# Optimization experiments

Hardware: AMD Instinct MI355X
Metric: run time of the kernel (lower is better)

Reference implementation:

```python
import jax, jax.numpy as jnp
import numpy as np

H = 1024      # hidden_size
L = 2         # num_layers
B = 4096      # batch_size (acts as sequential time axis)
IN = 33       # LSTM input size (17 raw + 8 ip-embed + 8 port-embed)


def setup_inputs() -> dict:
    key = jax.random.key(0)
    ks = jax.random.split(key, 16)
    s = 0.02
    return {
        "x": jax.random.normal(ks[0], (B, 17), dtype=jnp.float32),
        "ip": jax.random.randint(ks[1], (B, 8), 0, 256),
        "port": jax.random.randint(ks[2], (B, 2), 0, 70000),
        "hidden": jnp.zeros((L, 1, H), dtype=jnp.float32),
        "cell": jnp.zeros((L, 1, H), dtype=jnp.float32),
        "ip_emb": jax.random.normal(ks[3], (256, 1), dtype=jnp.float32) * s,
        "port_emb": jax.random.normal(ks[4], (70000, 4), dtype=jnp.float32) * s,
        "W_ih0": jax.random.normal(ks[5], (4 * H, IN), dtype=jnp.float32) * s,
        "W_hh0": jax.random.normal(ks[6], (4 * H, H), dtype=jnp.float32) * s,
        "b_ih0": jax.random.normal(ks[7], (4 * H,), dtype=jnp.float32) * s,
        "b_hh0": jax.random.normal(ks[8], (4 * H,), dtype=jnp.float32) * s,
        "W_ih1": jax.random.normal(ks[9], (4 * H, H), dtype=jnp.float32) * s,
        "W_hh1": jax.random.normal(ks[10], (4 * H, H), dtype=jnp.float32) * s,
        "b_ih1": jax.random.normal(ks[11], (4 * H,), dtype=jnp.float32) * s,
        "b_hh1": jax.random.normal(ks[12], (4 * H,), dtype=jnp.float32) * s,
    }


def reference(x, ip, port, hidden, cell, ip_emb, port_emb,
              W_ih0, W_hh0, b_ih0, b_hh0, W_ih1, W_hh1, b_ih1, b_hh1):
    # embedding lookups + concat -> [B, 33]
    ip_e = ip_emb[ip].reshape(B, -1)        # [B, 8]
    port_e = port_emb[port].reshape(B, -1)  # [B, 8]
    xin = jnp.concatenate((x, ip_e, port_e), axis=1)  # [B, 33]

    Wih = (W_ih0, W_ih1)
    Whh = (W_hh0, W_hh1)
    bih = (b_ih0, b_ih1)
    bhh = (b_hh0, b_hh1)

    h0 = hidden[:, 0]  # [L, H]
    c0 = cell[:, 0]    # [L, H]

    def step(carry, xt):
        h, c = carry
        inp = xt
        hs, cs = [], []
        for l in range(L):  # fixed small layer loop
            gates = Wih[l] @ inp + bih[l] + Whh[l] @ h[l] + bhh[l]  # [4H]
            i, f, g, o = jnp.split(gates, 4)  # PyTorch gate order: i,f,g,o
            i = jax.nn.sigmoid(i)
            f = jax.nn.sigmoid(f)
            g = jnp.tanh(g)
            o = jax.nn.sigmoid(o)
            c_new = f * c[l] + i * g
            h_new = o * jnp.tanh(c_new)
            hs.append(h_new)
            cs.append(c_new)
            inp = h_new
        return (jnp.stack(hs), jnp.stack(cs)), jax.nn.relu(inp)

    (hf, cf), outputs = jax.lax.scan(step, (h0, c0), xin)
    return outputs, (hf[:, None, :], cf[:, None, :])
```

## Files before the change

### kernel.cpp

```cpp
#include <hip/hip_runtime.h>
#include <hip/hip_fp16.h>
#include <math.h>

#define Hn 1024
#define Bn 4096
#define INW 33
#define OUTS (Bn * Hn)
#define TPB 512
#define ROWP 1024

typedef _Float16 half2v __attribute__((ext_vector_type(2)));
typedef unsigned uint4v __attribute__((ext_vector_type(4)));

__device__ __forceinline__ float sigmoidf_(float x) {
    return 1.0f / (1.0f + __expf(-x));
}
__device__ __forceinline__ float tanhf_(float x) {
    float e = __expf(-2.0f * fabsf(x));
    float r = (1.0f - e) / (1.0f + e);
    return copysignf(r, x);
}
__device__ __forceinline__ unsigned pack2(float a, float b) {
    __half2 h = __floats2half2_rn(a, b);
    return __builtin_bit_cast(unsigned, h);
}
__device__ __forceinline__ float dot2acc(unsigned w, unsigned hv, float acc) {
#if __has_builtin(__builtin_amdgcn_fdot2)
    return __builtin_amdgcn_fdot2(__builtin_bit_cast(half2v, w),
                                  __builtin_bit_cast(half2v, hv), acc, false);
#else
    __half2 wh = __builtin_bit_cast(__half2, w);
    __half2 hh = __builtin_bit_cast(__half2, hv);
    float2 wf = __half22float2(wh), hf = __half22float2(hh);
    return acc + wf.x * hf.x + wf.y * hf.y;
#endif
}

__device__ __forceinline__ unsigned spin_slice(const unsigned long long* slice,
                                               int lane, unsigned tag) {
    unsigned long long v;
    int rounds = 0;
    for (;;) {
        asm volatile("global_load_dwordx2 %0, %1, off sc0 sc1\n\t"
                     "s_waitcnt vmcnt(0)"
                     : "=v"(v) : "v"(slice + lane) : "memory");
        if (__all((unsigned)(v >> 32) == tag)) break;
        if (++rounds > (1 << 24)) break;
    }
    return (unsigned)v;
}

__device__ __forceinline__ void spin_slice2(const unsigned long long* sliceA,
                                            const unsigned long long* sliceB,
                                            int lane, unsigned tag,
                                            unsigned& dA, unsigned& dB) {
    unsigned long long va, vb;
    int rounds = 0;
    for (;;) {
        asm volatile("global_load_dwordx2 %0, %2, off sc0 sc1\n\t"
                     "global_load_dwordx2 %1, %3, off sc0 sc1\n\t"
                     "s_waitcnt vmcnt(0)"
                     : "=v"(va), "=v"(vb)
                     : "v"(sliceA + lane), "v"(sliceB + lane) : "memory");
        bool ok = ((unsigned)(va >> 32) == tag) & ((unsigned)(vb >> 32) == tag);
        if (__all(ok)) break;
        if (++rounds > (1 << 24)) break;
    }
    dA = (unsigned)va;
    dB = (unsigned)vb;
}

__device__ __forceinline__ void store16_coherent(void* dst, uint4v v) {
    asm volatile("global_store_dwordx4 %0, %1, off sc0 sc1"
                 :: "v"(dst), "v"(v) : "memory");
}
__device__ __forceinline__ void store8_coherent(void* dst, unsigned long long v) {
    asm volatile("global_store_dwordx2 %0, %1, off sc0 sc1"
                 :: "v"(dst), "v"(v) : "memory");
}

__global__ void prep_kernel(const float* __restrict__ x, const int* __restrict__ ip,
                            const int* __restrict__ port, const float* __restrict__ ip_emb,
                            const float* __restrict__ port_emb, float* __restrict__ xin) {
    int gid = blockIdx.x * blockDim.x + threadIdx.x;
    if (gid < Bn * INW) {
        int t = gid / INW;
        int k = gid - t * INW;
        float v;
        if (k < 17) {
            v = x[t * 17 + k];
        } else if (k < 25) {
            v = ip_emb[ip[t * 8 + (k - 17)]];
        } else {
            int kk = k - 25;
            v = port_emb[port[t * 2 + (kk >> 2)] * 4 + (kk & 3)];
        }
        xin[gid] = v;
    }
}

__global__ void __launch_bounds__(TPB, 2) lstm_kernel(
    const float* __restrict__ xin,
    const float* __restrict__ hid0, const float* __restrict__ cel0,
    const float* __restrict__ Wih0, const float* __restrict__ Whh0,
    const float* __restrict__ bih0, const float* __restrict__ bhh0,
    const float* __restrict__ Wih1, const float* __restrict__ Whh1,
    const float* __restrict__ bih1, const float* __restrict__ bhh1,
    float* __restrict__ out,
    unsigned long long* __restrict__ rowpkt)
{
    __shared__ unsigned hs2[2][1024];
    const int tid  = threadIdx.x;
    const int lane = tid & 63;
    const int wave = tid >> 6;
    const int bx   = blockIdx.x;

    if (bx < 32) {
        const int j0 = bx * 32 + wave * 4;
        unsigned w2[4][4][8];
        float    wx[4][4];
        float    bs[4][4];
#pragma unroll
        for (int jj = 0; jj < 4; ++jj) {
#pragma unroll
            for (int g = 0; g < 4; ++g) {
                const int row = g * Hn + (j0 + jj);
                const float* wr = Whh0 + (size_t)row * Hn;
#pragma unroll
                for (int k = 0; k < 8; ++k) {
                    int c = lane + 64 * k;
                    w2[jj][g][k] = pack2(wr[2 * c], wr[2 * c + 1]);
                }
                wx[jj][g] = (lane < INW) ? Wih0[row * INW + lane] : 0.0f;
                bs[jj][g] = bih0[row] + bhh0[row];
            }
        }
        float cst[4], hcur[4];
#pragma unroll
        for (int jj = 0; jj < 4; ++jj) { cst[jj] = cel0[j0 + jj]; hcur[jj] = 0.0f; }

        for (int s = 0; s < Bn; ++s) {
            const int b = s & 1;
            float xv = xin[s * INW + (lane < INW ? lane : 0)];
            if (s == 0) {
                int q = wave * 64 + lane;
                hs2[0][q] = pack2(hid0[2 * q], hid0[2 * q + 1]);
            } else {
                unsigned d = spin_slice(rowpkt + (size_t)(s - 1) * ROWP + wave * 64,
                                        lane, (unsigned)s);
                hs2[b][wave * 64 + lane] = d;
            }
            __syncthreads();

            float acc[4][4];
#pragma unroll
            for (int jj = 0; jj < 4; ++jj)
#pragma unroll
                for (int g = 0; g < 4; ++g) acc[jj][g] = wx[jj][g] * xv;
#pragma unroll
            for (int k = 0; k < 8; ++k) {
                unsigned hv = hs2[b][lane + 64 * k];
#pragma unroll
                for (int jj = 0; jj < 4; ++jj)
#pragma unroll
                    for (int g = 0; g < 4; ++g)
                        acc[jj][g] = dot2acc(w2[jj][g][k], hv, acc[jj][g]);
            }

#pragma unroll
            for (int off = 32; off >= 1; off >>= 1)
#pragma unroll
                for (int jj = 0; jj < 4; ++jj)
#pragma unroll
                    for (int g = 0; g < 4; ++g)
                        acc[jj][g] += __shfl_xor(acc[jj][g], off);

#pragma unroll
            for (int jj = 0; jj < 4; ++jj) {
                float gi = sigmoidf_(acc[jj][0] + bs[jj][0]);
                float gf = sigmoidf_(acc[jj][1] + bs[jj][1]);
                float gg = tanhf_   (acc[jj][2] + bs[jj][2]);
                float go = sigmoidf_(acc[jj][3] + bs[jj][3]);
                cst[jj] = gf * cst[jj] + gi * gg;
                hcur[jj] = go * tanhf_(cst[jj]);
            }
            if (lane == 0) {
                unsigned tag = (unsigned)(s + 1);
                uint4v v;
                v.x = pack2(hcur[0], hcur[1]);  v.y = tag;
                v.z = pack2(hcur[2], hcur[3]);  v.w = tag;
                char* dst = (char*)(rowpkt + (size_t)s * ROWP) + bx * 128 + wave * 16;
                store16_coherent(dst, v);
            }
        }
        if (lane == 0) {
#pragma unroll
            for (int jj = 0; jj < 4; ++jj) {
                out[OUTS + j0 + jj] = hcur[jj];
                out[OUTS + 2 * Hn + j0 + jj] = cst[jj];
            }
        }
    } else {
        const int blk = bx - 32;
        const int j0  = blk * 16 + wave * 2;
        unsigned w2[2][4][16];
        float    bs[2][4];
#pragma unroll
        for (int jj = 0; jj < 2; ++jj) {
#pragma unroll
            for (int g = 0; g < 4; ++g) {
                const int row = g * Hn + (j0 + jj);
                const float* wr1 = Wih1 + (size_t)row * Hn;
                const float* wr2 = Whh1 + (size_t)row * Hn;
#pragma unroll
                for (int k = 0; k < 8; ++k) {
                    int c = lane + 64 * k;
                    w2[jj][g][k]     = pack2(wr1[2 * c], wr1[2 * c + 1]);
                    w2[jj][g][8 + k] = pack2(wr2[2 * c], wr2[2 * c + 1]);
                }
                bs[jj][g] = bih1[row] + bhh1[row];
            }
        }
        float cst[2], hcur[2];
#pragma unroll
        for (int jj = 0; jj < 2; ++jj) { cst[jj] = cel0[Hn + j0 + jj]; hcur[jj] = 0.0f; }

        if (wave == 0 && lane < 4) {
            int base = Hn + blk * 16 + 4 * lane;
            uint4v v;
            v.x = pack2(hid0[base],     hid0[base + 1]);  v.y = 1u;
            v.z = pack2(hid0[base + 2], hid0[base + 3]);  v.w = 1u;
            char* dst = (char*)(rowpkt + 512) + blk * 64 + lane * 16;
            store16_coherent(dst, v);
        }

        for (int s = 1; s <= Bn; ++s) {
            const int t = s - 1;
            const int b = s & 1;
            const unsigned long long* rb = rowpkt + (size_t)(s - 1) * ROWP;
            unsigned dA, dB;
            spin_slice2(rb + wave * 64, rb + 512 + wave * 64, lane, (unsigned)s, dA, dB);
            hs2[b][wave * 64 + lane]       = dA;
            hs2[b][512 + wave * 64 + lane] = dB;
            __syncthreads();

            float acc[2][4];
#pragma unroll
            for (int jj = 0; jj < 2; ++jj)
#pragma unroll
                for (int g = 0; g < 4; ++g) acc[jj][g] = 0.0f;
#pragma unroll
            for (int k = 0; k < 16; ++k) {
                unsigned hv = hs2[b][lane + 64 * k];
#pragma unroll
                for (int jj = 0; jj < 2; ++jj)
#pragma unroll
                    for (int g = 0; g < 4; ++g)
                        acc[jj][g] = dot2acc(w2[jj][g][k], hv, acc[jj][g]);
            }

#pragma unroll
            for (int off = 32; off >= 1; off >>= 1)
#pragma unroll
                for (int jj = 0; jj < 2; ++jj)
#pragma unroll
                    for (int g = 0; g < 4; ++g)
                        acc[jj][g] += __shfl_xor(acc[jj][g], off);

#pragma unroll
            for (int jj = 0; jj < 2; ++jj) {
                float gi = sigmoidf_(acc[jj][0] + bs[jj][0]);
                float gf = sigmoidf_(acc[jj][1] + bs[jj][1]);
                float gg = tanhf_   (acc[jj][2] + bs[jj][2]);
                float go = sigmoidf_(acc[jj][3] + bs[jj][3]);
                cst[jj] = gf * cst[jj] + gi * gg;
                hcur[jj] = go * tanhf_(cst[jj]);
            }
            if (lane == 0) {
                unsigned long long pkt =
                    (((unsigned long long)(s + 1)) << 32) | pack2(hcur[0], hcur[1]);
                char* dst = (char*)(rowpkt + (size_t)s * ROWP + 512) + blk * 64 + wave * 8;
                store8_coherent(dst, pkt);
                float2 o2 = make_float2(fmaxf(hcur[0], 0.0f), fmaxf(hcur[1], 0.0f));
                *(float2*)(out + (size_t)t * Hn + j0) = o2;
            }
        }
        if (lane == 0) {
#pragma unroll
            for (int jj = 0; jj < 2; ++jj) {
                out[OUTS + Hn + j0 + jj] = hcur[jj];
                out[OUTS + 3 * Hn + j0 + jj] = cst[jj];
            }
        }
    }
}

extern "C" void kernel_launch(void* const* d_in, const int* in_sizes, int n_in,
                              void* d_out, int out_size, void* d_ws, size_t ws_size,
                              hipStream_t stream) {
    const float* x        = (const float*)d_in[0];
    const int*   ip       = (const int*)d_in[1];
    const int*   port     = (const int*)d_in[2];
    const float* hidden   = (const float*)d_in[3];
    const float* cell     = (const float*)d_in[4];
    const float* ip_emb   = (const float*)d_in[5];
    const float* port_emb = (const float*)d_in[6];
    const float* Wih0     = (const float*)d_in[7];
    const float* Whh0     = (const float*)d_in[8];
    const float* bih0     = (const float*)d_in[9];
    const float* bhh0     = (const float*)d_in[10];
    const float* Wih1     = (const float*)d_in[11];
    const float* Whh1     = (const float*)d_in[12];
    const float* bih1     = (const float*)d_in[13];
    const float* bhh1     = (const float*)d_in[14];
    float* out = (float*)d_out;

    unsigned long long* rowpkt = (unsigned long long*)d_ws;
    float* xin = (float*)(rowpkt + (size_t)(Bn + 1) * ROWP);

    prep_kernel<<<dim3((Bn * INW + 255) / 256), dim3(256), 0, stream>>>(
        x, ip, port, ip_emb, port_emb, xin);

    lstm_kernel<<<dim3(96), dim3(TPB), 0, stream>>>(
        xin, hidden, cell, Wih0, Whh0, bih0, bhh0, Wih1, Whh1, bih1, bhh1,
        out, rowpkt);
}
```

Before: 19.79 ms.

## Replace per-step packet array with 8-slot ring buffer and single-wave polling

```diff
diff --git a/kernel.cpp b/kernel.cpp
--- a/kernel.cpp
+++ b/kernel.cpp
@@ -7,10 +7,13 @@
 #define INW 33
 #define OUTS (Bn * Hn)
 #define TPB 512
-#define ROWP 1024
+#define ROW64 1024
+#define RSLOTS 8
+#define BAILOUT (1 << 22)
 
 typedef _Float16 half2v __attribute__((ext_vector_type(2)));
 typedef unsigned uint4v __attribute__((ext_vector_type(4)));
+
 
 __device__ __forceinline__ float sigmoidf_(float x) {
     return 1.0f / (1.0f + __expf(-x));
@@ -36,40 +39,6 @@
 #endif
 }
 
-__device__ __forceinline__ unsigned spin_slice(const unsigned long long* slice,
-                                               int lane, unsigned tag) {
-    unsigned long long v;
-    int rounds = 0;
-    for (;;) {
-        asm volatile("global_load_dwordx2 %0, %1, off sc0 sc1\n\t"
-                     "s_waitcnt vmcnt(0)"
-                     : "=v"(v) : "v"(slice + lane) : "memory");
-        if (__all((unsigned)(v >> 32) == tag)) break;
-        if (++rounds > (1 << 24)) break;
-    }
-    return (unsigned)v;
-}
-
-__device__ __forceinline__ void spin_slice2(const unsigned long long* sliceA,
-                                            const unsigned long long* sliceB,
-                                            int lane, unsigned tag,
-                                            unsigned& dA, unsigned& dB) {
-    unsigned long long va, vb;
-    int rounds = 0;
-    for (;;) {
-        asm volatile("global_load_dwordx2 %0, %2, off sc0 sc1\n\t"
-                     "global_load_dwordx2 %1, %3, off sc0 sc1\n\t"
-                     "s_waitcnt vmcnt(0)"
-                     : "=v"(va), "=v"(vb)
-                     : "v"(sliceA + lane), "v"(sliceB + lane) : "memory");
-        bool ok = ((unsigned)(va >> 32) == tag) & ((unsigned)(vb >> 32) == tag);
-        if (__all(ok)) break;
-        if (++rounds > (1 << 24)) break;
-    }
-    dA = (unsigned)va;
-    dB = (unsigned)vb;
-}
-
 __device__ __forceinline__ void store16_coherent(void* dst, uint4v v) {
     asm volatile("global_store_dwordx4 %0, %1, off sc0 sc1"
                  :: "v"(dst), "v"(v) : "memory");
@@ -77,6 +46,63 @@
 __device__ __forceinline__ void store8_coherent(void* dst, unsigned long long v) {
     asm volatile("global_store_dwordx2 %0, %1, off sc0 sc1"
                  :: "v"(dst), "v"(v) : "memory");
+}
+
+__device__ __forceinline__ void spin_half(const unsigned long long* hb, int lane,
+                                          unsigned tag, unsigned* dst) {
+    const unsigned long long* p = hb + 8 * lane;
+    uint4v q0, q1, q2, q3;
+    int rounds = 0;
+    for (;;) {
+        asm volatile(
+            "global_load_dwordx4 %0, %4, off sc0 sc1\n\t"
+            "global_load_dwordx4 %1, %4, off offset:16 sc0 sc1\n\t"
+            "global_load_dwordx4 %2, %4, off offset:32 sc0 sc1\n\t"
+            "global_load_dwordx4 %3, %4, off offset:48 sc0 sc1\n\t"
+            "s_waitcnt vmcnt(0)"
+            : "=v"(q0), "=v"(q1), "=v"(q2), "=v"(q3)
+            : "v"(p) : "memory");
+        bool ok = (q0.y == tag) & (q0.w == tag) & (q1.y == tag) & (q1.w == tag)
+                & (q2.y == tag) & (q2.w == tag) & (q3.y == tag) & (q3.w == tag);
+        if (__all(ok)) break;
+        if (++rounds > BAILOUT) break;
+    }
+    dst[8 * lane + 0] = q0.x;  dst[8 * lane + 1] = q0.z;
+    dst[8 * lane + 2] = q1.x;  dst[8 * lane + 3] = q1.z;
+    dst[8 * lane + 4] = q2.x;  dst[8 * lane + 5] = q2.z;
+    dst[8 * lane + 6] = q3.x;  dst[8 * lane + 7] = q3.z;
+}
+
+__device__ __forceinline__ void spin_l0_row(const unsigned long long* rb,
+                                            const unsigned long long* gb,
+                                            int lane, unsigned tag,
+                                            unsigned gtag, int use_gate,
+                                            unsigned* dst) {
+    const unsigned long long* p  = rb + 8 * lane;
+    const unsigned long long* gp = gb + 512 + 8 * lane;
+    uint4v q0, q1, q2, q3;
+    unsigned long long g;
+    int rounds = 0;
+    for (;;) {
+        asm volatile(
+            "global_load_dwordx4 %0, %5, off sc0 sc1\n\t"
+            "global_load_dwordx4 %1, %5, off offset:16 sc0 sc1\n\t"
+            "global_load_dwordx4 %2, %5, off offset:32 sc0 sc1\n\t"
+            "global_load_dwordx4 %3, %5, off offset:48 sc0 sc1\n\t"
+            "global_load_dwordx2 %4, %6, off sc0 sc1\n\t"
+            "s_waitcnt vmcnt(0)"
+            : "=v"(q0), "=v"(q1), "=v"(q2), "=v"(q3), "=v"(g)
+            : "v"(p), "v"(gp) : "memory");
+        bool ok = (q0.y == tag) & (q0.w == tag) & (q1.y == tag) & (q1.w == tag)
+                & (q2.y == tag) & (q2.w == tag) & (q3.y == tag) & (q3.w == tag);
+        if (use_gate) ok &= ((unsigned)(g >> 32) == gtag);
+        if (__all(ok)) break;
+        if (++rounds > BAILOUT) break;
+    }
+    dst[8 * lane + 0] = q0.x;  dst[8 * lane + 1] = q0.z;
+    dst[8 * lane + 2] = q1.x;  dst[8 * lane + 3] = q1.z;
+    dst[8 * lane + 4] = q2.x;  dst[8 * lane + 5] = q2.z;
+    dst[8 * lane + 6] = q3.x;  dst[8 * lane + 7] = q3.z;
 }
 
 __global__ void prep_kernel(const float* __restrict__ x, const int* __restrict__ ip,
@@ -107,7 +133,7 @@
     const float* __restrict__ Wih1, const float* __restrict__ Whh1,
     const float* __restrict__ bih1, const float* __restrict__ bhh1,
     float* __restrict__ out,
-    unsigned long long* __restrict__ rowpkt)
+    unsigned long long* __restrict__ ring)
 {
     __shared__ unsigned hs2[2][1024];
     const int tid  = threadIdx.x;
@@ -142,13 +168,21 @@
         for (int s = 0; s < Bn; ++s) {
             const int b = s & 1;
             float xv = xin[s * INW + (lane < INW ? lane : 0)];
-            if (s == 0) {
-                int q = wave * 64 + lane;
-                hs2[0][q] = pack2(hid0[2 * q], hid0[2 * q + 1]);
-            } else {
-                unsigned d = spin_slice(rowpkt + (size_t)(s - 1) * ROWP + wave * 64,
-                                        lane, (unsigned)s);
-                hs2[b][wave * 64 + lane] = d;
+            if (wave == 0) {
+                if (s == 0) {
+#pragma unroll
+                    for (int k = 0; k < 8; ++k) {
+                        int q = k * 64 + lane;
+                        hs2[0][q] = pack2(hid0[2 * q], hid0[2 * q + 1]);
+                    }
+                } else {
+                    const unsigned long long* rb =
+                        ring + (size_t)((s - 1) & (RSLOTS - 1)) * ROW64;
+                    const unsigned long long* gb =
+                        ring + (size_t)((s - 7) & (RSLOTS - 1)) * ROW64;
+                    spin_l0_row(rb, gb, lane, (unsigned)s,
+                                (unsigned)(s - 6), s >= 8, &hs2[b][0]);
+                }
             }
             __syncthreads();
 
@@ -185,12 +219,13 @@
                 hcur[jj] = go * tanhf_(cst[jj]);
             }
             if (lane == 0) {
-                unsigned tag = (unsigned)(s + 1);
+                unsigned tg = (unsigned)(s + 1);
                 uint4v v;
-                v.x = pack2(hcur[0], hcur[1]);  v.y = tag;
-                v.z = pack2(hcur[2], hcur[3]);  v.w = tag;
-                char* dst = (char*)(rowpkt + (size_t)s * ROWP) + bx * 128 + wave * 16;
-                store16_coherent(dst, v);
+                v.x = pack2(hcur[0], hcur[1]);  v.y = tg;
+                v.z = pack2(hcur[2], hcur[3]);  v.w = tg;
+                store16_coherent(
+                    (void*)(ring + (size_t)(s & (RSLOTS - 1)) * ROW64 + bx * 16 + wave * 2),
+                    v);
             }
         }
         if (lane == 0) {
@@ -225,23 +260,22 @@
 #pragma unroll
         for (int jj = 0; jj < 2; ++jj) { cst[jj] = cel0[Hn + j0 + jj]; hcur[jj] = 0.0f; }
 
-        if (wave == 0 && lane < 4) {
-            int base = Hn + blk * 16 + 4 * lane;
-            uint4v v;
-            v.x = pack2(hid0[base],     hid0[base + 1]);  v.y = 1u;
-            v.z = pack2(hid0[base + 2], hid0[base + 3]);  v.w = 1u;
-            char* dst = (char*)(rowpkt + 512) + blk * 64 + lane * 16;
-            store16_coherent(dst, v);
+        if (lane == 0) {
+            int base = Hn + blk * 16 + wave * 2;
+            unsigned long long pkt =
+                (1ull << 32) | pack2(hid0[base], hid0[base + 1]);
+            store8_coherent((void*)(ring + 512 + blk * 8 + wave), pkt);
         }
 
         for (int s = 1; s <= Bn; ++s) {
             const int t = s - 1;
             const int b = s & 1;
-            const unsigned long long* rb = rowpkt + (size_t)(s - 1) * ROWP;
-            unsigned dA, dB;
-            spin_slice2(rb + wave * 64, rb + 512 + wave * 64, lane, (unsigned)s, dA, dB);
-            hs2[b][wave * 64 + lane]       = dA;
-            hs2[b][512 + wave * 64 + lane] = dB;
+            const unsigned long long* rb =
+                ring + (size_t)((s - 1) & (RSLOTS - 1)) * ROW64;
+            if (wave == 0)
+                spin_half(rb,       lane, (unsigned)s, &hs2[b][0]);
+            else if (wave == 1)
+                spin_half(rb + 512, lane, (unsigned)s, &hs2[b][512]);
             __syncthreads();
 
             float acc[2][4];
@@ -279,8 +313,9 @@
             if (lane == 0) {
                 unsigned long long pkt =
                     (((unsigned long long)(s + 1)) << 32) | pack2(hcur[0], hcur[1]);
-                char* dst = (char*)(rowpkt + (size_t)s * ROWP + 512) + blk * 64 + wave * 8;
-                store8_coherent(dst, pkt);
+                store8_coherent(
+                    (void*)(ring + (size_t)(s & (RSLOTS - 1)) * ROW64 + 512 + blk * 8 + wave),
+                    pkt);
                 float2 o2 = make_float2(fmaxf(hcur[0], 0.0f), fmaxf(hcur[1], 0.0f));
                 *(float2*)(out + (size_t)t * Hn + j0) = o2;
             }
@@ -315,13 +350,13 @@
     const float* bhh1     = (const float*)d_in[14];
     float* out = (float*)d_out;
 
-    unsigned long long* rowpkt = (unsigned long long*)d_ws;
-    float* xin = (float*)(rowpkt + (size_t)(Bn + 1) * ROWP);
+    unsigned long long* ring = (unsigned long long*)d_ws;
+    float* xin = (float*)(ring + (size_t)RSLOTS * ROW64);
 
     prep_kernel<<<dim3((Bn * INW + 255) / 256), dim3(256), 0, stream>>>(
         x, ip, port, ip_emb, port_emb, xin);
 
     lstm_kernel<<<dim3(96), dim3(TPB), 0, stream>>>(
         xin, hidden, cell, Wih0, Whh0, bih0, bhh0, Wih1, Whh1, bih1, bhh1,
-        out, rowpkt);
-}
+        out, ring);
+}
```

Result: slower. 21.10 ms (+6.7%).
